# Kernel optimization log

Hardware: AMD Instinct MI355X
Metric: run time of the kernel (lower is better)

## Reference

```python
import jax, jax.numpy as jnp
import numpy as np

B, N, E = 2, 50000, 400000
FIN, HID, OUT = 128, 128, 128
EPS = 1e-5  # BatchNorm1d default eps


def setup_inputs() -> dict:
    key = jax.random.key(0)
    ks = jax.random.split(key, 12)
    x = jax.random.normal(ks[0], (B, N, FIN), dtype=jnp.float32)
    row = jax.random.randint(ks[1], (E,), 0, N, dtype=jnp.int32)          # scatter dst
    col = jnp.concatenate([jnp.arange(N, dtype=jnp.int32),                # ensure deg>=1
                           jax.random.randint(ks[2], (E - N,), 0, N, dtype=jnp.int32)])
    edge_index = jnp.stack([row, col])                                    # [2, E]
    deg = jnp.zeros((N,), jnp.float32).at[col].add(1.0)                   # degree(col, N)
    dis = deg ** -0.5
    norm = (dis[row] * dis[col])[None, :, None]                           # [1, E, 1]
    W1 = jax.random.normal(ks[3], (HID, FIN), jnp.float32) / np.sqrt(FIN)
    b1 = jax.random.normal(ks[4], (HID,), jnp.float32) * 0.01
    g1 = jnp.ones((N,), jnp.float32)
    be1 = jnp.zeros((N,), jnp.float32)
    W2 = jax.random.normal(ks[5], (OUT, HID), jnp.float32) / np.sqrt(HID)
    b2 = jax.random.normal(ks[6], (OUT,), jnp.float32) * 0.01
    g2 = jnp.ones((N,), jnp.float32)
    be2 = jnp.zeros((N,), jnp.float32)
    return {"x": x, "edge_index": edge_index, "norm": norm,
            "W1": W1, "b1": b1, "g1": g1, "be1": be1,
            "W2": W2, "b2": b2, "g2": g2, "be2": be2}


def _gcn_layer(x, edge_index, norm, W, b, g, be):
    # Linear (dropout p=0 -> identity)
    h = jnp.einsum('bnf,of->bno', x, W) + b                 # [B, N, C]
    # BatchNorm1d(num_features=N): per-node stats over (batch, channel)
    mu = jnp.mean(h, axis=(0, 2), keepdims=True)            # [1, N, 1]
    var = jnp.var(h, axis=(0, 2), keepdims=True)            # biased, as torch
    y = g[None, :, None] * (h - mu) * jax.lax.rsqrt(var + EPS) + be[None, :, None]
    a = jax.nn.gelu(y, approximate=False)                   # torch GELU = exact erf
    # message passing: gather src nodes, scale by norm, scatter-add to dst
    msgs = a[:, edge_index[1], :] * norm                    # [B, E, C]
    return jnp.zeros_like(a).at[:, edge_index[0], :].add(msgs)


def reference(x, edge_index, norm, W1, b1, g1, be1, W2, b2, g2, be2):
    x = _gcn_layer(x, edge_index, norm, W1, b1, g1, be1)
    x = _gcn_layer(x, edge_index, norm, W2, b2, g2, be2)
    return x
```

## Files before the change

### kernel.cpp

```cpp
#include <hip/hip_runtime.h>
#include <math.h>

#define CC 128
#define TPAD 132

typedef unsigned short u16;
typedef short bf16x8 __attribute__((ext_vector_type(8)));
typedef short bf16x4 __attribute__((ext_vector_type(4)));
typedef float f32x4 __attribute__((ext_vector_type(4)));

__device__ __forceinline__ u16 f2bf(float f) {
    union { float f; unsigned u; } v; v.f = f;
    unsigned u = v.u;
    return (u16)((u + 0x7FFFu + ((u >> 16) & 1u)) >> 16);
}
__device__ __forceinline__ float bf2f(unsigned hi16) {
    union { unsigned u; float f; } v; v.u = hi16 << 16; return v.f;
}

__device__ __forceinline__ float gelu_f(float y) {
    float xa = fabsf(y) * 0.70710678118654752f;
    float t  = __builtin_amdgcn_rcpf(fmaf(0.3275911f, xa, 1.0f));
    float p  = fmaf(1.061405429f, t, -1.453152027f);
    p = fmaf(p, t, 1.421413741f);
    p = fmaf(p, t, -0.284496736f);
    p = fmaf(p, t, 0.254829592f);
    p *= t;
    float e  = __expf(-xa * xa);
    float er = fmaf(-p, e, 1.0f);
    float s  = copysignf(er, y);
    return 0.5f * y * (1.0f + s);
}


__global__ __launch_bounds__(256) void k_zero_i32(int* __restrict__ p, int n) {
    int i = blockIdx.x * 256 + threadIdx.x;
    if (i < n) p[i] = 0;
}

__global__ __launch_bounds__(256) void k_hist(const int* __restrict__ row, int* __restrict__ cnt, int E) {
    int e = blockIdx.x * 256 + threadIdx.x;
    if (e < E) atomicAdd(&cnt[row[e]], 1);
}

__device__ __forceinline__ int wave_incl_scan(int v) {
    #pragma unroll
    for (int d = 1; d < 64; d <<= 1) {
        int t = __shfl_up(v, d);
        if ((threadIdx.x & 63) >= d) v += t;
    }
    return v;
}

__global__ __launch_bounds__(256) void k_scan_a(const int* __restrict__ cnt, int* __restrict__ bsum, int N) {
    int base = blockIdx.x * 1024 + threadIdx.x * 4;
    int s = 0;
    #pragma unroll
    for (int u = 0; u < 4; ++u) { int i = base + u; if (i < N) s += cnt[i]; }
    #pragma unroll
    for (int d = 32; d > 0; d >>= 1) s += __shfl_down(s, d);
    __shared__ int wsum[4];
    if ((threadIdx.x & 63) == 0) wsum[threadIdx.x >> 6] = s;
    __syncthreads();
    if (threadIdx.x == 0) bsum[blockIdx.x] = wsum[0] + wsum[1] + wsum[2] + wsum[3];
}

__global__ __launch_bounds__(64) void k_scan_b(const int* __restrict__ bsum, int* __restrict__ boff,
                                               int* __restrict__ off, int N, int nb) {
    int carry = 0;
    for (int base = 0; base < nb; base += 64) {
        int t = base + (int)threadIdx.x;
        int v = (t < nb) ? bsum[t] : 0;
        int incl = wave_incl_scan(v);
        if (t < nb) boff[t] = carry + incl - v;
        carry += __shfl(incl, 63);
    }
    if (threadIdx.x == 0) off[N] = carry;
}

__global__ __launch_bounds__(256) void k_scan_c(int* __restrict__ cnt, const int* __restrict__ boff,
                                                int* __restrict__ off, int N) {
    int t = threadIdx.x;
    int base = blockIdx.x * 1024 + t * 4;
    int v[4]; int s = 0;
    #pragma unroll
    for (int u = 0; u < 4; ++u) { int i = base + u; v[u] = (i < N) ? cnt[i] : 0; s += v[u]; }
    int incl = wave_incl_scan(s);
    __shared__ int wsum[4];
    int w = t >> 6, lane = t & 63;
    if (lane == 63) wsum[w] = incl;
    __syncthreads();
    int run = incl - s + boff[blockIdx.x];
    for (int ww = 0; ww < w; ++ww) run += wsum[ww];
    #pragma unroll
    for (int u = 0; u < 4; ++u) {
        int i = base + u;
        if (i < N) { off[i] = run; cnt[i] = 0; }
        run += v[u];
    }
}

__global__ __launch_bounds__(256) void k_fill(const int* __restrict__ row, const int* __restrict__ col,
                                              const float* __restrict__ nrm, const int* __restrict__ off,
                                              int* __restrict__ cur, int2* __restrict__ eg, int E) {
    int e = blockIdx.x * 256 + threadIdx.x;
    if (e < E) {
        int r = row[e];
        int p = off[r] + atomicAdd(&cur[r], 1);
        eg[p] = make_int2(col[e], __float_as_int(nrm[e]));
    }
}

__global__ __launch_bounds__(256) void k_wrepack(const float* __restrict__ W1, u16* __restrict__ Wp1,
                                                 const float* __restrict__ W2, u16* __restrict__ Wp2) {
    int i = blockIdx.x * 256 + threadIdx.x;
    const float* W = (i < CC * CC) ? W1 : W2;
    u16* Wp = (i < CC * CC) ? Wp1 : Wp2;
    int ii = (i < CC * CC) ? i : i - CC * CC;
    if (ii < CC * CC) {
        int j = ii & 7, l = (ii >> 3) & 63, s = (ii >> 9) & 3, t = ii >> 11;
        int r = 16 * t + (l & 15);
        int k = s * 32 + (l >> 4) * 8 + j;
        Wp[ii] = f2bf(W[r * CC + k]);
    }
}

template<int IN_BF16>
__global__ __launch_bounds__(256, 1) void k_gemm_bn_gelu(
    const void* __restrict__ Xv, const u16* __restrict__ Wp,
    const float* __restrict__ bias, const float* __restrict__ gamma, const float* __restrict__ beta,
    u16* __restrict__ Out, int N)
{
    __shared__ u16 T[4][16][TPAD];

    const int tid = threadIdx.x;
    const int w = tid >> 6;
    const int l = tid & 63;
    const int g = l >> 4;
    const int c = l & 15;
    const int n8 = blockIdx.x * 32 + w * 8;
    const bool valid = n8 < N;
    const int nbase = valid ? n8 : 0;

    bf16x8 B[32];
    #pragma unroll
    for (int i = 0; i < 32; ++i)
        B[i] = *(const bf16x8*)(Wp + ((size_t)i * 64 + l) * 8);

    const int ab = c >> 3;
    const int an = nbase + (c & 7);

    bf16x8 af[4];
    if (IN_BF16) {
        const u16* X = (const u16*)Xv;
        const u16* base = X + ((size_t)ab * N + an) * CC + g * 8;
        #pragma unroll
        for (int s = 0; s < 4; ++s) af[s] = *(const bf16x8*)(base + s * 32);
    } else {
        const float* X = (const float*)Xv;
        const float* base = X + ((size_t)ab * N + an) * CC + g * 8;
        float4 lo[4], hi[4];
        #pragma unroll
        for (int s = 0; s < 4; ++s) {
            lo[s] = *(const float4*)(base + s * 32);
            hi[s] = *(const float4*)(base + s * 32 + 4);
        }
        #pragma unroll
        for (int s = 0; s < 4; ++s) {
            bf16x8 v;
            v[0] = (short)f2bf(lo[s].x); v[1] = (short)f2bf(lo[s].y);
            v[2] = (short)f2bf(lo[s].z); v[3] = (short)f2bf(lo[s].w);
            v[4] = (short)f2bf(hi[s].x); v[5] = (short)f2bf(hi[s].y);
            v[6] = (short)f2bf(hi[s].z); v[7] = (short)f2bf(hi[s].w);
            af[s] = v;
        }
    }

    float bb[8];
    #pragma unroll
    for (int t = 0; t < 8; ++t) bb[t] = bias[t * 16 + c];
    float gam[4], bet[4];
    #pragma unroll
    for (int r = 0; r < 4; ++r) {
        int p = (4 * g + r) & 7;
        gam[r] = gamma[nbase + p];
        bet[r] = beta[nbase + p];
    }

    __builtin_amdgcn_sched_barrier(0);

    f32x4 acc[8];
    #pragma unroll
    for (int t = 0; t < 8; ++t) acc[t] = (f32x4){0.f, 0.f, 0.f, 0.f};

    #pragma unroll
    for (int s = 0; s < 4; ++s)
        #pragma unroll
        for (int t = 0; t < 8; ++t)
            acc[t] = __builtin_amdgcn_mfma_f32_16x16x32_bf16(af[s], B[t * 4 + s], acc[t], 0, 0, 0);

    float rs[4] = {0.f, 0.f, 0.f, 0.f}, rq[4] = {0.f, 0.f, 0.f, 0.f};
    #pragma unroll
    for (int t = 0; t < 8; ++t)
        #pragma unroll
        for (int r = 0; r < 4; ++r) {
            float h = acc[t][r] + bb[t];
            acc[t][r] = h;
            rs[r] += h;
            rq[r] += h * h;
        }
    #pragma unroll
    for (int d = 1; d < 16; d <<= 1) {
        #pragma unroll
        for (int r = 0; r < 4; ++r) {
            rs[r] += __shfl_xor(rs[r], d);
            rq[r] += __shfl_xor(rq[r], d);
        }
    }
    #pragma unroll
    for (int r = 0; r < 4; ++r) {
        rs[r] += __shfl_xor(rs[r], 32);
        rq[r] += __shfl_xor(rq[r], 32);
    }

    float sc[4], sh[4];
    #pragma unroll
    for (int r = 0; r < 4; ++r) {
        float mean = rs[r] * (1.f / 256.f);
        float var  = rq[r] * (1.f / 256.f) - mean * mean;
        float s_ = gam[r] * rsqrtf(fmaxf(var, 0.f) + 1e-5f);
        sc[r] = s_;
        sh[r] = bet[r] - mean * s_;
    }

    #pragma unroll
    for (int r = 0; r < 4; ++r) {
        int row = 4 * g + r;
        #pragma unroll
        for (int t = 0; t < 8; ++t) {
            float y = acc[t][r] * sc[r] + sh[r];
            T[w][row][t * 16 + c] = f2bf(gelu_f(y));
        }
    }
    __syncthreads();

    if (valid) {
        #pragma unroll
        for (int it = 0; it < 4; ++it) {
            int chunk = it * 64 + l;
            int rowi = chunk >> 4;
            int offc = (chunk & 15) * 8;
            int db = rowi >> 3;
            int dn = n8 + (rowi & 7);
            bf16x4 lo = *(const bf16x4*)&T[w][rowi][offc];
            bf16x4 hi = *(const bf16x4*)&T[w][rowi][offc + 4];
            bf16x8 v;
            v[0] = lo[0]; v[1] = lo[1]; v[2] = lo[2]; v[3] = lo[3];
            v[4] = hi[0]; v[5] = hi[1]; v[6] = hi[2]; v[7] = hi[3];
            *(bf16x8*)(Out + ((size_t)db * N + dn) * CC + offc) = v;
        }
    }
}

template<int OUT_F32>
__global__ __launch_bounds__(256) void k_aggregate(
    const u16* __restrict__ A, const int* __restrict__ off,
    const int2* __restrict__ eg, void* __restrict__ Outv, int N)
{
    int n = blockIdx.x * 4 + (threadIdx.x >> 6);
    if (n >= N) return;
    int l = threadIdx.x & 63;
    int p = l >> 5;
    int b = (l >> 4) & 1;
    int ch0 = (l & 15) * 8;
    const u16* Ab = A + (size_t)b * N * CC + ch0;
    int s = off[n], e = off[n + 1];
    float a[8] = {0.f, 0.f, 0.f, 0.f, 0.f, 0.f, 0.f, 0.f};
    for (int j = s; j < e; j += 8) {
        int i0 = j + p, i1 = j + 2 + p, i2 = j + 4 + p, i3 = j + 6 + p;
        int2 e0 = (i0 < e) ? eg[i0] : make_int2(0, 0);
        int2 e1 = (i1 < e) ? eg[i1] : make_int2(0, 0);
        int2 e2 = (i2 < e) ? eg[i2] : make_int2(0, 0);
        int2 e3 = (i3 < e) ? eg[i3] : make_int2(0, 0);
        bf16x8 v0 = *(const bf16x8*)(Ab + (size_t)e0.x * CC);
        bf16x8 v1 = *(const bf16x8*)(Ab + (size_t)e1.x * CC);
        bf16x8 v2 = *(const bf16x8*)(Ab + (size_t)e2.x * CC);
        bf16x8 v3 = *(const bf16x8*)(Ab + (size_t)e3.x * CC);
        float w0 = __int_as_float(e0.y), w1 = __int_as_float(e1.y);
        float w2 = __int_as_float(e2.y), w3 = __int_as_float(e3.y);
        #pragma unroll
        for (int q = 0; q < 8; ++q) {
            a[q] = fmaf(w0, bf2f((u16)v0[q]), a[q]);
            a[q] = fmaf(w1, bf2f((u16)v1[q]), a[q]);
            a[q] = fmaf(w2, bf2f((u16)v2[q]), a[q]);
            a[q] = fmaf(w3, bf2f((u16)v3[q]), a[q]);
        }
    }
    #pragma unroll
    for (int q = 0; q < 8; ++q) a[q] += __shfl_xor(a[q], 32);
    if (l < 32) {
        if (OUT_F32) {
            float* d = (float*)Outv + ((size_t)b * N + n) * CC + ch0;
            *(float4*)&d[0] = make_float4(a[0], a[1], a[2], a[3]);
            *(float4*)&d[4] = make_float4(a[4], a[5], a[6], a[7]);
        } else {
            u16* d = (u16*)Outv + ((size_t)b * N + n) * CC + ch0;
            bf16x8 v;
            #pragma unroll
            for (int q = 0; q < 8; ++q) v[q] = (short)f2bf(a[q]);
            *(bf16x8*)d = v;
        }
    }
}


extern "C" void kernel_launch(void* const* d_in, const int* in_sizes, int n_in,
                              void* d_out, int out_size, void* d_ws, size_t ws_size,
                              hipStream_t stream)
{
    const float* x   = (const float*)d_in[0];
    const int*   ei  = (const int*)d_in[1];
    const float* nrm = (const float*)d_in[2];
    const float* W1  = (const float*)d_in[3];
    const float* b1  = (const float*)d_in[4];
    const float* g1  = (const float*)d_in[5];
    const float* be1 = (const float*)d_in[6];
    const float* W2  = (const float*)d_in[7];
    const float* b2  = (const float*)d_in[8];
    const float* g2  = (const float*)d_in[9];
    const float* be2 = (const float*)d_in[10];

    const int N = in_sizes[5];
    const int E = in_sizes[2];
    const int* row = ei;
    const int* col = ei + E;
    const int nb = (N + 1023) / 1024;

    auto al = [](size_t v) { return (v + 255) & ~(size_t)255; };
    char* p = (char*)d_ws;
    int* off    = (int*)p;   p += al((size_t)(N + 1) * 4);
    int* cur    = (int*)p;   p += al((size_t)N * 4);
    int2* eg    = (int2*)p;  p += al((size_t)E * 8);
    int* bsum   = (int*)p;   p += al((size_t)nb * 4);
    int* boff   = (int*)p;   p += al((size_t)nb * 4);
    u16* Wp1    = (u16*)p;   p += al((size_t)CC * CC * 2);
    u16* Wp2    = (u16*)p;   p += al((size_t)CC * CC * 2);
    u16* bufA   = (u16*)p;   p += al((size_t)2 * N * CC * 2);
    u16* bufB   = (u16*)p;   p += al((size_t)2 * N * CC * 2);

    k_zero_i32<<<(N + 255) / 256, 256, 0, stream>>>(cur, N);
    k_hist<<<(E + 255) / 256, 256, 0, stream>>>(row, cur, E);
    k_scan_a<<<nb, 256, 0, stream>>>(cur, bsum, N);
    k_scan_b<<<1, 64, 0, stream>>>(bsum, boff, off, N, nb);
    k_scan_c<<<nb, 256, 0, stream>>>(cur, boff, off, N);
    k_fill<<<(E + 255) / 256, 256, 0, stream>>>(row, col, nrm, off, cur, eg, E);

    k_wrepack<<<(2 * CC * CC + 255) / 256, 256, 0, stream>>>(W1, Wp1, W2, Wp2);

    const int gb = (N + 31) / 32;
    const int ga = (N + 3) / 4;
    k_gemm_bn_gelu<0><<<gb, 256, 0, stream>>>(x, Wp1, b1, g1, be1, bufA, N);
    k_aggregate<0><<<ga, 256, 0, stream>>>(bufA, off, eg, bufB, N);
    k_gemm_bn_gelu<1><<<gb, 256, 0, stream>>>(bufB, Wp2, b2, g2, be2, bufA, N);
    k_aggregate<1><<<ga, 256, 0, stream>>>(bufA, off, eg, (float*)d_out, N);
}
```

Before: 175.7 us.

## Stage GEMM weights in LDS via direct global-to-LDS loads and raise occupancy

Instead of every wave loading the full 128x128 bf16 weight matrix into 32 vector registers, each block copies it once into 32KB of shared memory using global_load_lds and streams the B fragments from LDS per k-step. This frees many VGPRs, so launch bounds move from 1 to 4 blocks per SM to raise occupancy and hide memory latency. The LDS buffer is reused as the transpose staging area after an extra barrier. In exchange it adds LDS read traffic and two block-wide syncs per block.

Measured after the change: 169.9 us. 1.03x faster.

```diff
diff --git a/kernel.cpp b/kernel.cpp
--- a/kernel.cpp
+++ b/kernel.cpp
@@ -8,6 +8,9 @@
 typedef short bf16x8 __attribute__((ext_vector_type(8)));
 typedef short bf16x4 __attribute__((ext_vector_type(4)));
 typedef float f32x4 __attribute__((ext_vector_type(4)));
+
+typedef __attribute__((address_space(3))) void lds_t;
+typedef const __attribute__((address_space(1))) void gbl_t;
 
 __device__ __forceinline__ u16 f2bf(float f) {
     union { float f; unsigned u; } v; v.f = f;
@@ -126,12 +129,12 @@
 }
 
 template<int IN_BF16>
-__global__ __launch_bounds__(256, 1) void k_gemm_bn_gelu(
+__global__ __launch_bounds__(256, 4) void k_gemm_bn_gelu(
     const void* __restrict__ Xv, const u16* __restrict__ Wp,
     const float* __restrict__ bias, const float* __restrict__ gamma, const float* __restrict__ beta,
     u16* __restrict__ Out, int N)
 {
-    __shared__ u16 T[4][16][TPAD];
+    __shared__ __align__(16) u16 SM[CC * CC];
 
     const int tid = threadIdx.x;
     const int w = tid >> 6;
@@ -142,10 +145,12 @@
     const bool valid = n8 < N;
     const int nbase = valid ? n8 : 0;
 
-    bf16x8 B[32];
-    #pragma unroll
-    for (int i = 0; i < 32; ++i)
-        B[i] = *(const bf16x8*)(Wp + ((size_t)i * 64 + l) * 8);
+    #pragma unroll
+    for (int it = 0; it < 8; ++it) {
+        const u16* gsrc = Wp + it * 2048 + w * 512 + l * 8;
+        u16* ldst = &SM[it * 2048 + w * 512];
+        __builtin_amdgcn_global_load_lds((gbl_t*)gsrc, (lds_t*)ldst, 16, 0, 0);
+    }
 
     const int ab = c >> 3;
     const int an = nbase + (c & 7);
@@ -187,17 +192,22 @@
         bet[r] = beta[nbase + p];
     }
 
-    __builtin_amdgcn_sched_barrier(0);
+    __syncthreads();
 
     f32x4 acc[8];
     #pragma unroll
     for (int t = 0; t < 8; ++t) acc[t] = (f32x4){0.f, 0.f, 0.f, 0.f};
 
     #pragma unroll
-    for (int s = 0; s < 4; ++s)
+    for (int s = 0; s < 4; ++s) {
+        bf16x8 bf[8];
         #pragma unroll
         for (int t = 0; t < 8; ++t)
-            acc[t] = __builtin_amdgcn_mfma_f32_16x16x32_bf16(af[s], B[t * 4 + s], acc[t], 0, 0, 0);
+            bf[t] = *(const bf16x8*)&SM[((t * 4 + s) * 64 + l) * 8];
+        #pragma unroll
+        for (int t = 0; t < 8; ++t)
+            acc[t] = __builtin_amdgcn_mfma_f32_16x16x32_bf16(af[s], bf[t], acc[t], 0, 0, 0);
+    }
 
     float rs[4] = {0.f, 0.f, 0.f, 0.f}, rq[4] = {0.f, 0.f, 0.f, 0.f};
     #pragma unroll
@@ -233,16 +243,18 @@
         sh[r] = bet[r] - mean * s_;
     }
 
+    __syncthreads();
+
+    u16 (*T)[TPAD] = (u16 (*)[TPAD])(SM + w * 16 * TPAD);
     #pragma unroll
     for (int r = 0; r < 4; ++r) {
         int row = 4 * g + r;
         #pragma unroll
         for (int t = 0; t < 8; ++t) {
             float y = acc[t][r] * sc[r] + sh[r];
-            T[w][row][t * 16 + c] = f2bf(gelu_f(y));
-        }
-    }
-    __syncthreads();
+            T[row][t * 16 + c] = f2bf(gelu_f(y));
+        }
+    }
 
     if (valid) {
         #pragma unroll
@@ -252,8 +264,8 @@
             int offc = (chunk & 15) * 8;
             int db = rowi >> 3;
             int dn = n8 + (rowi & 7);
-            bf16x4 lo = *(const bf16x4*)&T[w][rowi][offc];
-            bf16x4 hi = *(const bf16x4*)&T[w][rowi][offc + 4];
+            bf16x4 lo = *(const bf16x4*)&T[rowi][offc];
+            bf16x4 hi = *(const bf16x4*)&T[rowi][offc + 4];
             bf16x8 v;
             v[0] = lo[0]; v[1] = lo[1]; v[2] = lo[2]; v[3] = lo[3];
             v[4] = hi[0]; v[5] = hi[1]; v[6] = hi[2]; v[7] = hi[3];
```
